# Kernel tuning notes

Hardware: AMD Instinct MI355X
Metric: run time of the kernel (lower is better)

The kernel has to match this reference:

```python
import jax, jax.numpy as jnp
import numpy as np

EMBED_DIM = 1024
NUM_HEADS = 16
HEAD_DIM = EMBED_DIM // NUM_HEADS
BATCH = 2
SEQ = 2048


def setup_inputs() -> dict:
    key = jax.random.key(0)
    ks = jax.random.split(key, 9)
    s = EMBED_DIM ** -0.5
    inp = {"x": jax.random.normal(ks[0], (BATCH, SEQ, EMBED_DIM), dtype=jnp.float32)}
    names = ["Wq", "Wk", "Wv", "Wo"]
    for i, n in enumerate(names):
        inp[n] = jax.random.normal(ks[1 + i], (EMBED_DIM, EMBED_DIM), dtype=jnp.float32) * s
        inp["b" + n[1]] = jax.random.normal(ks[5 + i], (EMBED_DIM,), dtype=jnp.float32) * 0.02
    return inp


def reference(x, Wq, bq, Wk, bk, Wv, bv, Wo, bo):
    B, S, E = x.shape
    H, D = NUM_HEADS, HEAD_DIM
    scaling = D ** -0.5
    # projections (torch Linear: x @ W.T + b), reshape to (B, H, S, D)
    q = (x @ Wq.T + bq).reshape(B, S, H, D).transpose(0, 2, 1, 3)
    k = (x @ Wk.T + bk).reshape(B, S, H, D).transpose(0, 2, 1, 3)
    v = (x @ Wv.T + bv).reshape(B, S, H, D).transpose(0, 2, 1, 3)
    # full materialized score matrix, matching the original module
    scores = jnp.einsum("bhqd,bhkd->bhqk", q, k) * scaling
    causal = jnp.triu(jnp.ones((S, S), dtype=bool), k=1)  # True above diagonal
    scores = jnp.where(causal[None, None], -jnp.inf, scores)
    attn = jax.nn.softmax(scores, axis=-1)
    out = jnp.einsum("bhqk,bhkd->bhqd", attn, v)  # (B, H, S, D)
    out = out.transpose(0, 2, 1, 3).reshape(B, S, E)
    return out @ Wo.T + bo
```

## Files before the change

kernel.cpp:

```cpp
#include <hip/hip_runtime.h>
#include <stdint.h>

typedef __bf16 bf16;
typedef __bf16 bf16x8 __attribute__((ext_vector_type(8)));
typedef __bf16 bf16x4 __attribute__((ext_vector_type(4)));
typedef float  f32x4  __attribute__((ext_vector_type(4)));
typedef unsigned int u32;

#define E_DIM 1024
#define S_LEN 2048
#define BATCH 2
#define NH 16
#define DH 64

#define NEG_INF (-__builtin_inff())

union BU { u32 u[4]; bf16x8 h; };

__device__ __forceinline__ u32 cvtpk_bf16(float lo, float hi) {
    u32 r;
    asm("v_cvt_pk_bf16_f32 %0, %1, %2" : "=v"(r) : "v"(lo), "v"(hi));
    return r;
}
__device__ __forceinline__ void pswap32(u32 &a, u32 &b) {
    asm("v_permlane32_swap_b32 %0, %1" : "+v"(a), "+v"(b));
}
__device__ __forceinline__ void pswap16(u32 &a, u32 &b) {
    asm("v_permlane16_swap_b32 %0, %1" : "+v"(a), "+v"(b));
}

__device__ __forceinline__ void load_lds16(const bf16* g, bf16* l) {
    __builtin_amdgcn_global_load_lds(
        (const __attribute__((address_space(1))) void*)g,
        (__attribute__((address_space(3))) void*)l, 16, 0, 0);
}

__global__ __launch_bounds__(256) void convert_kernel(
    const float* __restrict__ s0, const float* __restrict__ s1,
    const float* __restrict__ s2, const float* __restrict__ s3,
    const float* __restrict__ s4,
    bf16* __restrict__ d0, bf16* __restrict__ d1, bf16* __restrict__ d2,
    bf16* __restrict__ d3, bf16* __restrict__ d4,
    int n0, int n1)
{
    const float* src; bf16* dst; int n;
    switch (blockIdx.y) {
        case 0:  src = s0; dst = d0; n = n0; break;
        case 1:  src = s1; dst = d1; n = n1; break;
        case 2:  src = s2; dst = d2; n = n1; break;
        case 3:  src = s3; dst = d3; n = n1; break;
        default: src = s4; dst = d4; n = n1; break;
    }
    int i = (blockIdx.x * 256 + threadIdx.x) * 4;
    if (i >= n) return;
    float4 v = *(const float4*)(src + i);
    bf16x4 o;
    o[0] = (bf16)v.x; o[1] = (bf16)v.y; o[2] = (bf16)v.z; o[3] = (bf16)v.w;
    *(bf16x4*)(dst + i) = o;
}

__global__ __launch_bounds__(256) void gemm_kernel(
    const bf16* __restrict__ A,
    const bf16* __restrict__ W0, const bf16* __restrict__ W1, const bf16* __restrict__ W2,
    const float* __restrict__ bias0, const float* __restrict__ bias1, const float* __restrict__ bias2,
    bf16* __restrict__ outQ, bf16* __restrict__ outK, bf16* __restrict__ outVt,
    float* __restrict__ outF, int final_mode)
{
    __shared__ bf16 As[2][128 * 32];
    __shared__ bf16 Bs[2][128 * 32];

    int mode;
    const bf16* W; const float* bias;
    if (final_mode) { mode = 3; W = W0; bias = bias0; }
    else {
        mode = blockIdx.z;
        W    = (mode == 0) ? W0 : (mode == 1 ? W1 : W2);
        bias = (mode == 0) ? bias0 : (mode == 1 ? bias1 : bias2);
    }

    const int bm = blockIdx.y * 128, bn = blockIdx.x * 128;
    const int t = threadIdx.x;
    const int lane = t & 63, w = t >> 6;
    const int quad = lane >> 4, l16 = lane & 15;
    const int wm = (w & 1) * 64, wn = (w >> 1) * 64;

    const int r0 = w * 16;
    const int srow = r0 + (lane >> 2), scol = (lane & 3) * 8;
    const bf16* Ag0 = A + (size_t)(bm + srow) * E_DIM + scol;
    const bf16* Ag1 = Ag0 + (size_t)64 * E_DIM;
    const bf16* Wg0 = W + (size_t)(bn + srow) * E_DIM + scol;
    const bf16* Wg1 = Wg0 + (size_t)64 * E_DIM;

    f32x4 acc[4][4];
#pragma unroll
    for (int i = 0; i < 4; i++)
#pragma unroll
        for (int j = 0; j < 4; j++) acc[i][j] = f32x4{0.f, 0.f, 0.f, 0.f};

    load_lds16(Ag0, As[0] + r0 * 32);
    load_lds16(Ag1, As[0] + (64 + r0) * 32);
    load_lds16(Wg0, Bs[0] + r0 * 32);
    load_lds16(Wg1, Bs[0] + (64 + r0) * 32);

    int cur = 0;
    for (int kt = 0; kt < E_DIM; kt += 32) {
        __syncthreads();

        if (kt + 32 < E_DIM) {
            const int nxt = cur ^ 1;
            load_lds16(Ag0 + kt + 32, As[nxt] + r0 * 32);
            load_lds16(Ag1 + kt + 32, As[nxt] + (64 + r0) * 32);
            load_lds16(Wg0 + kt + 32, Bs[nxt] + r0 * 32);
            load_lds16(Wg1 + kt + 32, Bs[nxt] + (64 + r0) * 32);
        }

        bf16x8 af[4], bfr[4];
#pragma unroll
        for (int i = 0; i < 4; i++)
            af[i] = *(const bf16x8*)(As[cur] + (wm + i * 16 + l16) * 32 + quad * 8);
#pragma unroll
        for (int j = 0; j < 4; j++)
            bfr[j] = *(const bf16x8*)(Bs[cur] + (wn + j * 16 + l16) * 32 + quad * 8);
#pragma unroll
        for (int i = 0; i < 4; i++)
#pragma unroll
            for (int j = 0; j < 4; j++)
                acc[i][j] = __builtin_amdgcn_mfma_f32_16x16x32_bf16(af[i], bfr[j], acc[i][j], 0, 0, 0);

        cur ^= 1;
    }

#pragma unroll
    for (int j = 0; j < 4; j++) {
        const int n = bn + wn + j * 16 + l16;
        const float bv = bias[n];
#pragma unroll
        for (int i = 0; i < 4; i++) {
            const int m0 = bm + wm + i * 16 + quad * 4;
            if (mode == 3) {
#pragma unroll
                for (int r = 0; r < 4; r++)
                    outF[(size_t)(m0 + r) * E_DIM + n] = acc[i][j][r] + bv;
            } else if (mode == 2) {
                const int b_ = m0 >> 11, s0 = m0 & (S_LEN - 1);
                const int h = n >> 6, d = n & 63;
                bf16x4 pv;
#pragma unroll
                for (int r = 0; r < 4; r++) pv[r] = (bf16)(acc[i][j][r] + bv);
                *(bf16x4*)(outVt + ((size_t)((b_ * NH + h) * DH + d)) * S_LEN + s0) = pv;
            } else {
                bf16* o = (mode == 0) ? outQ : outK;
                const float sc = (mode == 0) ? 0.18033688f : 1.0f;
                const int h = n >> 6, d = n & 63;
#pragma unroll
                for (int r = 0; r < 4; r++) {
                    const int m = m0 + r;
                    const int b_ = m >> 11, s = m & (S_LEN - 1);
                    o[((size_t)(b_ * NH + h) * S_LEN + s) * DH + d] = (bf16)((acc[i][j][r] + bv) * sc);
                }
            }
        }
    }
}

__global__ __launch_bounds__(512, 4) void attn_kernel(
    const bf16* __restrict__ Qb, const bf16* __restrict__ Kb,
    const bf16* __restrict__ Vtb, bf16* __restrict__ Ob)
{
    __shared__ __align__(16) char smem[35840];
    bf16* Ks = (bf16*)smem;
    bf16* Vs = (bf16*)(smem + 18432);

    const int t = threadIdx.x, lane = t & 63, w = t >> 6;
    const int quad = lane >> 4, l16 = lane & 15;
    const int qs = w & 3, kh = w >> 2;

    const int i = blockIdx.x;
    const int half = i >> 8, jj = i & 255;
    const int xcd = jj & 7, rr = jj >> 3;
    const int bh = (xcd << 2) | (rr & 3);
    const int qq = rr >> 2;
    const int qt = half ? qq : 15 - qq;

    const bf16* Qg = Qb + (size_t)bh * S_LEN * DH;
    const bf16* Kg = Kb + (size_t)bh * S_LEN * DH;
    const bf16* Vg = Vtb + (size_t)bh * DH * S_LEN;
    const int b_ = bh >> 4, hh = bh & 15;
    bf16* Og = Ob + (size_t)b_ * S_LEN * E_DIM + hh * DH;

    const int qrow0 = qt * 128 + qs * 32;

    bf16x8 qf[2][2];
#pragma unroll
    for (int qh = 0; qh < 2; qh++) {
        const bf16* qp = Qg + (size_t)(qrow0 + qh * 16 + l16) * DH + quad * 8;
        qf[qh][0] = *(const bf16x8*)(qp);
        qf[qh][1] = *(const bf16x8*)(qp + 32);
    }

    f32x4 o[2][4];
    f32x4 lacc[2];
#pragma unroll
    for (int qh = 0; qh < 2; qh++) {
        lacc[qh] = f32x4{0.f, 0.f, 0.f, 0.f};
#pragma unroll
        for (int dt = 0; dt < 4; dt++) o[qh][dt] = f32x4{0.f, 0.f, 0.f, 0.f};
    }

    const int T = qt + 1;
    const int kr0 = t >> 3, kce = (t & 7) * 8;
    const int vr0 = t >> 4, vce = (t & 15) * 8;

    uint4 k0 = *(const uint4*)(Kg + (size_t)kr0 * DH + kce);
    uint4 k1 = *(const uint4*)(Kg + (size_t)(kr0 + 64) * DH + kce);
    uint4 v0 = *(const uint4*)(Vg + (size_t)vr0 * S_LEN + vce);
    uint4 v1 = *(const uint4*)(Vg + (size_t)(vr0 + 32) * S_LEN + vce);

    for (int kt = 0; kt < T; kt++) {
        __syncthreads();
        *(uint4*)(Ks + kr0 * 72 + kce) = k0;
        *(uint4*)(Ks + (kr0 + 64) * 72 + kce) = k1;
        *(uint4*)(Vs + vr0 * 136 + vce) = v0;
        *(uint4*)(Vs + (vr0 + 32) * 136 + vce) = v1;
        __syncthreads();

        if (kt + 1 < T) {
            const int kb = (kt + 1) * 128;
            k0 = *(const uint4*)(Kg + (size_t)(kb + kr0) * DH + kce);
            k1 = *(const uint4*)(Kg + (size_t)(kb + kr0 + 64) * DH + kce);
            v0 = *(const uint4*)(Vg + (size_t)vr0 * S_LEN + kb + vce);
            v1 = *(const uint4*)(Vg + (size_t)(vr0 + 32) * S_LEN + kb + vce);
        }

        const bool diag = (kt == qt);

#pragma unroll
        for (int itp = 0; itp < 2; itp++) {
            f32x4 p[2][2];
#pragma unroll
            for (int e = 0; e < 2; e++) {
                const int itg = kh * 4 + itp * 2 + e;
                const bf16* kp = Ks + (itg * 16 + l16) * 72 + quad * 8;
                bf16x8 kf0 = *(const bf16x8*)(kp);
                bf16x8 kf1 = *(const bf16x8*)(kp + 32);
#pragma unroll
                for (int qh = 0; qh < 2; qh++) {
                    f32x4 s = __builtin_amdgcn_mfma_f32_16x16x32_bf16(
                        kf0, qf[qh][0], f32x4{0.f, 0.f, 0.f, 0.f}, 0, 0, 0);
                    s = __builtin_amdgcn_mfma_f32_16x16x32_bf16(
                        kf1, qf[qh][1], s, 0, 0, 0);
                    if (diag) {
                        const int kloc = kh * 64 + (itp * 2 + e) * 16 + quad * 4;
                        const int qloc = qs * 32 + qh * 16 + l16;
#pragma unroll
                        for (int r = 0; r < 4; r++)
                            if (kloc + r > qloc) s[r] = NEG_INF;
                    }
                    f32x4 pe;
#pragma unroll
                    for (int r = 0; r < 4; r++) pe[r] = exp2f(s[r]);
                    lacc[qh] += pe;
                    p[qh][e] = pe;
                }
            }

            BU bu0, bu1;
            {
                u32 a0 = cvtpk_bf16(p[0][0][0], p[0][0][1]);
                u32 a1 = cvtpk_bf16(p[0][0][2], p[0][0][3]);
                u32 b0 = cvtpk_bf16(p[0][1][0], p[0][1][1]);
                u32 b1 = cvtpk_bf16(p[0][1][2], p[0][1][3]);
                pswap32(a0, b0); pswap16(a0, b0);
                pswap32(a1, b1); pswap16(a1, b1);
                bu0.u[0] = a0; bu0.u[1] = a1; bu0.u[2] = b0; bu0.u[3] = b1;
            }
            {
                u32 a0 = cvtpk_bf16(p[1][0][0], p[1][0][1]);
                u32 a1 = cvtpk_bf16(p[1][0][2], p[1][0][3]);
                u32 b0 = cvtpk_bf16(p[1][1][0], p[1][1][1]);
                u32 b1 = cvtpk_bf16(p[1][1][2], p[1][1][3]);
                pswap32(a0, b0); pswap16(a0, b0);
                pswap32(a1, b1); pswap16(a1, b1);
                bu1.u[0] = a0; bu1.u[1] = a1; bu1.u[2] = b0; bu1.u[3] = b1;
            }

            const int ksg = kh * 2 + itp;
#pragma unroll
            for (int dt = 0; dt < 4; dt++) {
                bf16x8 vf = *(const bf16x8*)(Vs + (dt * 16 + l16) * 136 + ksg * 32 + quad * 8);
                o[0][dt] = __builtin_amdgcn_mfma_f32_16x16x32_bf16(vf, bu0.h, o[0][dt], 0, 0, 0);
                o[1][dt] = __builtin_amdgcn_mfma_f32_16x16x32_bf16(vf, bu1.h, o[1][dt], 0, 0, 0);
            }
        }
    }

    float lsum[2];
#pragma unroll
    for (int qh = 0; qh < 2; qh++) {
        float l = lacc[qh][0] + lacc[qh][1] + lacc[qh][2] + lacc[qh][3];
        l += __shfl_xor(l, 16);
        l += __shfl_xor(l, 32);
        lsum[qh] = l;
    }

    __syncthreads();
    f32x4* Or = (f32x4*)smem;
    float*  Lr = (float*)(smem + 32768);

    if (kh == 1) {
#pragma unroll
        for (int qh = 0; qh < 2; qh++) {
#pragma unroll
            for (int dt = 0; dt < 4; dt++)
                Or[(((qs * 2 + qh) * 4 + dt) * 4 + quad) * 16 + l16] = o[qh][dt];
            if (quad == 0) Lr[(qs * 2 + qh) * 16 + l16] = lsum[qh];
        }
    }
    __syncthreads();
    if (kh == 0) {
#pragma unroll
        for (int qh = 0; qh < 2; qh++) {
            const float inv = 1.0f / (lsum[qh] + Lr[(qs * 2 + qh) * 16 + l16]);
            const int qg = qrow0 + qh * 16 + l16;
#pragma unroll
            for (int dt = 0; dt < 4; dt++) {
                f32x4 ov = o[qh][dt] + Or[(((qs * 2 + qh) * 4 + dt) * 4 + quad) * 16 + l16];
                bf16x4 w4;
#pragma unroll
                for (int r = 0; r < 4; r++) w4[r] = (bf16)(ov[r] * inv);
                *(bf16x4*)(Og + (size_t)qg * E_DIM + dt * 16 + quad * 4) = w4;
            }
        }
    }
}

extern "C" void kernel_launch(void* const* d_in, const int* in_sizes, int n_in,
                              void* d_out, int out_size, void* d_ws, size_t ws_size,
                              hipStream_t stream)
{
    const float* x  = (const float*)d_in[0];
    const float* Wq = (const float*)d_in[1];
    const float* bq = (const float*)d_in[2];
    const float* Wk = (const float*)d_in[3];
    const float* bk = (const float*)d_in[4];
    const float* Wv = (const float*)d_in[5];
    const float* bv = (const float*)d_in[6];
    const float* Wo = (const float*)d_in[7];
    const float* bo = (const float*)d_in[8];
    float* out = (float*)d_out;

    char* ws = (char*)d_ws;
    const size_t MB = 1ull << 20;
    bf16* xb  = (bf16*)(ws + 0);
    bf16* wqb = (bf16*)(ws + 8 * MB);
    bf16* wkb = (bf16*)(ws + 10 * MB);
    bf16* wvb = (bf16*)(ws + 12 * MB);
    bf16* wob = (bf16*)(ws + 14 * MB);
    bf16* Qb  = (bf16*)(ws + 16 * MB);
    bf16* Kb  = (bf16*)(ws + 24 * MB);
    bf16* Vtb = (bf16*)(ws + 32 * MB);
    bf16* Ab  = (bf16*)(ws + 40 * MB);

    convert_kernel<<<dim3(4096, 5), 256, 0, stream>>>(
        x, Wq, Wk, Wv, Wo, xb, wqb, wkb, wvb, wob, 4194304, 1048576);

    gemm_kernel<<<dim3(8, 32, 3), 256, 0, stream>>>(
        xb, wqb, wkb, wvb, bq, bk, bv, Qb, Kb, Vtb, nullptr, 0);

    attn_kernel<<<dim3(512), 512, 0, stream>>>(Qb, Kb, Vtb, Ab);

    gemm_kernel<<<dim3(8, 32, 1), 256, 0, stream>>>(
        Ab, wob, wob, wob, bo, bo, bo, nullptr, nullptr, nullptr, out, 1);
}
```

Measured before the change: 193.3 us.

## Split attention over key-tile chunks with atomic fp32 accumulation and separate normalize

Each causal query tile's key range is split into chunks of at most four key tiles, giving 1280 blocks that each do a bounded amount of work. Because the softmax uses no running max, partial numerators and denominators can simply be summed, so each block atomically adds them into zero-initialised fp32 buffers. A new norm kernel then divides and converts the result to bf16, and the convert kernel gains an extra slice that zeroes the buffers. exp2f is also replaced with a raw v_exp_f32. The aim is better load balance and occupancy; the cost is many global float atomics, an extra launch and 16 MB of extra fp32 traffic.

```diff
diff --git a/kernel.cpp b/kernel.cpp
--- a/kernel.cpp
+++ b/kernel.cpp
@@ -27,6 +27,11 @@
 }
 __device__ __forceinline__ void pswap16(u32 &a, u32 &b) {
     asm("v_permlane16_swap_b32 %0, %1" : "+v"(a), "+v"(b));
+}
+__device__ __forceinline__ float fast_exp2(float x) {
+    float r;
+    asm("v_exp_f32 %0, %1" : "=v"(r) : "v"(x));
+    return r;
 }
 
 __device__ __forceinline__ void load_lds16(const bf16* g, bf16* l) {
@@ -41,8 +46,16 @@
     const float* __restrict__ s4,
     bf16* __restrict__ d0, bf16* __restrict__ d1, bf16* __restrict__ d2,
     bf16* __restrict__ d3, bf16* __restrict__ d4,
+    float* __restrict__ Oacc, float* __restrict__ Lacc,
     int n0, int n1)
 {
+    if (blockIdx.y == 5) {
+        const int i = (blockIdx.x * 256 + threadIdx.x) * 4;
+        *(f32x4*)(Oacc + i) = f32x4{0.f, 0.f, 0.f, 0.f};
+        if (blockIdx.x < 64)
+            *(f32x4*)(Lacc + i) = f32x4{0.f, 0.f, 0.f, 0.f};
+        return;
+    }
     const float* src; bf16* dst; int n;
     switch (blockIdx.y) {
         case 0:  src = s0; dst = d0; n = n0; break;
@@ -165,7 +178,8 @@
 
 __global__ __launch_bounds__(512, 4) void attn_kernel(
     const bf16* __restrict__ Qb, const bf16* __restrict__ Kb,
-    const bf16* __restrict__ Vtb, bf16* __restrict__ Ob)
+    const bf16* __restrict__ Vtb,
+    float* __restrict__ Oacc, float* __restrict__ Lacc)
 {
     __shared__ __align__(16) char smem[35840];
     bf16* Ks = (bf16*)smem;
@@ -176,17 +190,22 @@
     const int qs = w & 3, kh = w >> 2;
 
     const int i = blockIdx.x;
-    const int half = i >> 8, jj = i & 255;
-    const int xcd = jj & 7, rr = jj >> 3;
-    const int bh = (xcd << 2) | (rr & 3);
-    const int qq = rr >> 2;
-    const int qt = half ? qq : 15 - qq;
+    const int xcd = i & 7, idx = i >> 3;
+    const int bh  = (xcd << 2) | (idx & 3);
+    const int g   = idx >> 2;
+    int qt, c0;
+    if (g < 4)       { qt = g;                            c0 = 0; }
+    else if (g < 12) { int u = g - 4;  qt = 4 + (u >> 1); c0 = u & 1; }
+    else if (g < 24) { int u = g - 12; qt = 8 + u / 3;    c0 = u % 3; }
+    else             { int u = g - 24; qt = 12 + (u >> 2); c0 = u & 3; }
+    const int k0 = c0 * 4;
+    const int k1 = (k0 + 3 < qt) ? k0 + 3 : qt;
 
     const bf16* Qg = Qb + (size_t)bh * S_LEN * DH;
     const bf16* Kg = Kb + (size_t)bh * S_LEN * DH;
     const bf16* Vg = Vtb + (size_t)bh * DH * S_LEN;
-    const int b_ = bh >> 4, hh = bh & 15;
-    bf16* Og = Ob + (size_t)b_ * S_LEN * E_DIM + hh * DH;
+    float* Oa = Oacc + (size_t)bh * S_LEN * DH;
+    float* La = Lacc + (size_t)bh * S_LEN;
 
     const int qrow0 = qt * 128 + qs * 32;
 
@@ -207,29 +226,29 @@
         for (int dt = 0; dt < 4; dt++) o[qh][dt] = f32x4{0.f, 0.f, 0.f, 0.f};
     }
 
-    const int T = qt + 1;
     const int kr0 = t >> 3, kce = (t & 7) * 8;
     const int vr0 = t >> 4, vce = (t & 15) * 8;
 
-    uint4 k0 = *(const uint4*)(Kg + (size_t)kr0 * DH + kce);
-    uint4 k1 = *(const uint4*)(Kg + (size_t)(kr0 + 64) * DH + kce);
-    uint4 v0 = *(const uint4*)(Vg + (size_t)vr0 * S_LEN + vce);
-    uint4 v1 = *(const uint4*)(Vg + (size_t)(vr0 + 32) * S_LEN + vce);
-
-    for (int kt = 0; kt < T; kt++) {
+    const int kb0 = k0 * 128;
+    uint4 kA = *(const uint4*)(Kg + (size_t)(kb0 + kr0) * DH + kce);
+    uint4 kB = *(const uint4*)(Kg + (size_t)(kb0 + kr0 + 64) * DH + kce);
+    uint4 vA = *(const uint4*)(Vg + (size_t)vr0 * S_LEN + kb0 + vce);
+    uint4 vB = *(const uint4*)(Vg + (size_t)(vr0 + 32) * S_LEN + kb0 + vce);
+
+    for (int kt = k0; kt <= k1; kt++) {
         __syncthreads();
-        *(uint4*)(Ks + kr0 * 72 + kce) = k0;
-        *(uint4*)(Ks + (kr0 + 64) * 72 + kce) = k1;
-        *(uint4*)(Vs + vr0 * 136 + vce) = v0;
-        *(uint4*)(Vs + (vr0 + 32) * 136 + vce) = v1;
+        *(uint4*)(Ks + kr0 * 72 + kce) = kA;
+        *(uint4*)(Ks + (kr0 + 64) * 72 + kce) = kB;
+        *(uint4*)(Vs + vr0 * 136 + vce) = vA;
+        *(uint4*)(Vs + (vr0 + 32) * 136 + vce) = vB;
         __syncthreads();
 
-        if (kt + 1 < T) {
+        if (kt < k1) {
             const int kb = (kt + 1) * 128;
-            k0 = *(const uint4*)(Kg + (size_t)(kb + kr0) * DH + kce);
-            k1 = *(const uint4*)(Kg + (size_t)(kb + kr0 + 64) * DH + kce);
-            v0 = *(const uint4*)(Vg + (size_t)vr0 * S_LEN + kb + vce);
-            v1 = *(const uint4*)(Vg + (size_t)(vr0 + 32) * S_LEN + kb + vce);
+            kA = *(const uint4*)(Kg + (size_t)(kb + kr0) * DH + kce);
+            kB = *(const uint4*)(Kg + (size_t)(kb + kr0 + 64) * DH + kce);
+            vA = *(const uint4*)(Vg + (size_t)vr0 * S_LEN + kb + vce);
+            vB = *(const uint4*)(Vg + (size_t)(vr0 + 32) * S_LEN + kb + vce);
         }
 
         const bool diag = (kt == qt);
@@ -258,7 +277,7 @@
                     }
                     f32x4 pe;
 #pragma unroll
-                    for (int r = 0; r < 4; r++) pe[r] = exp2f(s[r]);
+                    for (int r = 0; r < 4; r++) pe[r] = fast_exp2(s[r]);
                     lacc[qh] += pe;
                     p[qh][e] = pe;
                 }
@@ -320,18 +339,34 @@
     if (kh == 0) {
 #pragma unroll
         for (int qh = 0; qh < 2; qh++) {
-            const float inv = 1.0f / (lsum[qh] + Lr[(qs * 2 + qh) * 16 + l16]);
+            const float lc = lsum[qh] + Lr[(qs * 2 + qh) * 16 + l16];
             const int qg = qrow0 + qh * 16 + l16;
+            if (quad == 0) atomicAdd(&La[qg], lc);
 #pragma unroll
             for (int dt = 0; dt < 4; dt++) {
                 f32x4 ov = o[qh][dt] + Or[(((qs * 2 + qh) * 4 + dt) * 4 + quad) * 16 + l16];
-                bf16x4 w4;
-#pragma unroll
-                for (int r = 0; r < 4; r++) w4[r] = (bf16)(ov[r] * inv);
-                *(bf16x4*)(Og + (size_t)qg * E_DIM + dt * 16 + quad * 4) = w4;
-            }
-        }
-    }
+                float* op = Oa + (size_t)qg * DH + dt * 16 + quad * 4;
+#pragma unroll
+                for (int r = 0; r < 4; r++) atomicAdd(op + r, ov[r]);
+            }
+        }
+    }
+}
+
+__global__ __launch_bounds__(256) void norm_kernel(
+    const float* __restrict__ Oacc, const float* __restrict__ Lacc,
+    bf16* __restrict__ Ab)
+{
+    const int j = (blockIdx.x * 256 + threadIdx.x) * 4;
+    const int b = j >> 21, s = (j >> 10) & (S_LEN - 1), e = j & 1023;
+    const int h = e >> 6, d = e & 63;
+    const size_t bhs = (size_t)(b * NH + h) * S_LEN + s;
+    const float inv = 1.0f / Lacc[bhs];
+    f32x4 ov = *(const f32x4*)(Oacc + bhs * DH + d);
+    bf16x4 w4;
+#pragma unroll
+    for (int r = 0; r < 4; r++) w4[r] = (bf16)(ov[r] * inv);
+    *(bf16x4*)(Ab + j) = w4;
 }
 
 extern "C" void kernel_launch(void* const* d_in, const int* in_sizes, int n_in,
@@ -351,23 +386,27 @@
 
     char* ws = (char*)d_ws;
     const size_t MB = 1ull << 20;
-    bf16* xb  = (bf16*)(ws + 0);
-    bf16* wqb = (bf16*)(ws + 8 * MB);
-    bf16* wkb = (bf16*)(ws + 10 * MB);
-    bf16* wvb = (bf16*)(ws + 12 * MB);
-    bf16* wob = (bf16*)(ws + 14 * MB);
-    bf16* Qb  = (bf16*)(ws + 16 * MB);
-    bf16* Kb  = (bf16*)(ws + 24 * MB);
-    bf16* Vtb = (bf16*)(ws + 32 * MB);
-    bf16* Ab  = (bf16*)(ws + 40 * MB);
-
-    convert_kernel<<<dim3(4096, 5), 256, 0, stream>>>(
-        x, Wq, Wk, Wv, Wo, xb, wqb, wkb, wvb, wob, 4194304, 1048576);
+    bf16*  xb   = (bf16*)(ws + 0);
+    bf16*  wqb  = (bf16*)(ws + 8 * MB);
+    bf16*  wkb  = (bf16*)(ws + 10 * MB);
+    bf16*  wvb  = (bf16*)(ws + 12 * MB);
+    bf16*  wob  = (bf16*)(ws + 14 * MB);
+    bf16*  Qb   = (bf16*)(ws + 16 * MB);
+    bf16*  Kb   = (bf16*)(ws + 24 * MB);
+    bf16*  Vtb  = (bf16*)(ws + 32 * MB);
+    bf16*  Ab   = (bf16*)(ws + 40 * MB);
+    float* Oacc = (float*)(ws + 48 * MB);
+    float* Lacc = (float*)(ws + 64 * MB);
+
+    convert_kernel<<<dim3(4096, 6), 256, 0, stream>>>(
+        x, Wq, Wk, Wv, Wo, xb, wqb, wkb, wvb, wob, Oacc, Lacc, 4194304, 1048576);
 
     gemm_kernel<<<dim3(8, 32, 3), 256, 0, stream>>>(
         xb, wqb, wkb, wvb, bq, bk, bv, Qb, Kb, Vtb, nullptr, 0);
 
-    attn_kernel<<<dim3(512), 512, 0, stream>>>(Qb, Kb, Vtb, Ab);
+    attn_kernel<<<dim3(1280), 512, 0, stream>>>(Qb, Kb, Vtb, Oacc, Lacc);
+
+    norm_kernel<<<dim3(4096), 256, 0, stream>>>(Oacc, Lacc, Ab);
 
     gemm_kernel<<<dim3(8, 32, 1), 256, 0, stream>>>(
         Ab, wob, wob, wob, bo, bo, bo, nullptr, nullptr, nullptr, out, 1);
```

After: 296.6 us. 1.53x slower.
